# Kernel optimization log

Hardware: AMD Instinct MI355X
Metric: run time of the kernel (lower is better)

Reference implementation:

```python
import jax, jax.numpy as jnp
import numpy as np

B, C_IN, N = 128, 256, 1024
C_OUT = 256
L = 3069  # 3 * (N - 1) triplet indices, multiple of kernel_size=3


def setup_inputs() -> dict:
    key = jax.random.key(0)
    k1, k2, k3, k4 = jax.random.split(key, 4)
    data = jax.random.normal(k1, (B, C_IN, N), dtype=jnp.float32)
    indexes = jax.random.randint(k2, (B, L, 1), 0, N, dtype=jnp.int64)
    # Conv1d(in_dims, out_dims, kernel_size=3) params, PyTorch layout [out, in, k]
    fan_in = C_IN * 3
    bound = 1.0 / np.sqrt(fan_in)
    weight = jax.random.uniform(k3, (C_OUT, C_IN, 3), dtype=jnp.float32, minval=-bound, maxval=bound)
    bias = jax.random.uniform(k4, (C_OUT,), dtype=jnp.float32, minval=-bound, maxval=bound)
    return {"data": data, "indexes": indexes, "weight": weight, "bias": bias}


def reference(data, indexes, weight, bias):
    # gather: data[b, c, indexes[b, l, 0]] -> [B, C_IN, L]
    idx = indexes[:, :, 0]  # [B, L]
    gathered = jnp.take_along_axis(data, idx[:, None, :], axis=2)  # broadcast over channel dim
    # Conv1d kernel_size=3 stride=3 == per-triplet matmul:
    # reshape [B, C_IN, L] -> [B, C_IN, L//3, 3]; contract with weight [C_OUT, C_IN, 3]
    trip = gathered.reshape(B, gathered.shape[1], L // 3, 3)
    feats = jnp.einsum('bcnk,ock->bon', trip, weight) + bias[None, :, None]  # [B, C_OUT, L//3]
    # prepend a zero column (padding slot for node index 0)
    zeros = jnp.zeros((feats.shape[0], feats.shape[1], 1), dtype=feats.dtype)
    feats = jnp.concatenate((zeros, feats), axis=2)  # [B, C_OUT, L//3 + 1]
    return (feats, indexes)
```

## Files before the change

### kernel.cpp

```cpp
#include <hip/hip_runtime.h>

#define B_      128
#define C_IN_   256
#define NPTS    1024
#define C_OUT_  256
#define L_      3069
#define NTRIP   1023
#define T_OUT   1024
#define FEATS_SIZE (B_ * C_OUT_ * T_OUT)
#define KTOT    768

#define BK      96
#define NCHUNK  8
#define THREADS 512

typedef __attribute__((ext_vector_type(8))) short           bf16x8;
typedef __attribute__((ext_vector_type(8))) unsigned short  ushort8;
typedef __attribute__((ext_vector_type(4))) unsigned short  ushort4v;
typedef __attribute__((ext_vector_type(4))) float           f32x4;

__device__ __forceinline__ unsigned short f2bf(float f) {
    union { float f; unsigned u; } v; v.f = f;
    unsigned r = (v.u + 0x7FFFu + ((v.u >> 16) & 1u)) >> 16;
    return (unsigned short)r;
}

#define WOFF_T  0
#define DOFF_T  393216
#define WS_NEED_T2 (393216 + 67108864)

#define IDX3    32768
#define SMEM3   34304
#define BN2     128

__global__ __launch_bounds__(256) void convert_w3(
    const float* __restrict__ w, unsigned short* __restrict__ wbf3)
{
    int i = blockIdx.x * 256 + threadIdx.x;
    if (i >= C_OUT_ * KTOT) return;
    int j   = i & 7;
    int lgv = (i >> 3) & 3;
    int row = (i >> 5) & 255;
    int c   = i >> 13;
    int ks  = c % 3;
    int kc  = c / 3;
    int korig = (kc * 32 + lgv * 8 + j) * 3 + ks;
    wbf3[i] = f2bf(w[row * KTOT + korig]);
}

__global__ __launch_bounds__(256) void transpose_data(
    const float* __restrict__ data, unsigned short* __restrict__ dataT)
{
    __shared__ float T[64][68];
    const int bid = blockIdx.x;
    const int b   = bid >> 6;
    const int ct  = (bid & 63) >> 4;
    const int nt  = bid & 15;
    const int c0  = ct * 64, n0 = nt * 64;
    const int t   = threadIdx.x;
    const int row = t >> 2;
    const int q   = t & 3;

    const float* src = data + ((size_t)(b * C_IN_ + c0 + row)) * NPTS + n0 + q * 16;
    #pragma unroll
    for (int j = 0; j < 4; ++j) {
        float4 v = *(const float4*)(src + j * 4);
        *(float4*)&T[row][q * 16 + j * 4] = v;
    }
    __syncthreads();

    ushort8 o0, o1;
    #pragma unroll
    for (int j = 0; j < 8; ++j)  o0[j] = f2bf(T[q * 16 + j][row]);
    #pragma unroll
    for (int j = 0; j < 8; ++j)  o1[j] = f2bf(T[q * 16 + 8 + j][row]);
    unsigned short* dst = dataT + ((size_t)(b * NPTS) + n0 + row) * C_IN_ + c0 + q * 16;
    *(ushort8*)(dst)     = o0;
    *(ushort8*)(dst + 8) = o1;
}

__global__ __launch_bounds__(THREADS, 4) void treeconv_mfma3(
    const unsigned short* __restrict__ wbf3,
    const unsigned short* __restrict__ dataT,
    const int*   __restrict__ indexes,
    const float* __restrict__ bias,
    float*       __restrict__ out)
{
    __shared__ alignas(16) unsigned char smem[SMEM3];
    int* idx_s = (int*)(smem + IDX3);

    const int tid = threadIdx.x;
    const int b   = blockIdx.x >> 3;
    const int nt0 = (blockIdx.x & 7) * BN2;

    if (tid < BN2 * 3) {
        int off = nt0 * 3 + tid;
        idx_s[tid] = (off < L_) ? indexes[b * L_ + off] : 0;
    }
    __syncthreads();

    const int lane = tid & 63;
    const int wid  = tid >> 6;
    const int wm   = wid >> 1;
    const int wn   = wid & 1;
    const int l15  = lane & 15;
    const int lg   = lane >> 4;

    unsigned boff[4];
    #pragma unroll
    for (int j = 0; j < 4; ++j) {
        int slot = wid * 256 + j * 64 + lane;
        int n    = slot >> 4;
        int el   = (slot & 15) ^ (n & 7);
        int tap  = (el < 12) ? (el >> 2) : 0;
        int q    = el & 3;
        int ix   = idx_s[n * 3 + tap];
        boff[j]  = (unsigned)(ix * (C_IN_ * 2) + q * 16);
    }

    const char* dTb  = (const char*)dataT + (size_t)b * NPTS * C_IN_ * 2;
    const char* wsrc = (const char*)wbf3;
    const int   aoff = wm * 4096 + l15 * 64 + lg * 16;
    unsigned char* bdst = smem + wid * 4096 + lane * 16;

    f32x4 acc[4][4];
    #pragma unroll
    for (int mi = 0; mi < 4; ++mi)
        #pragma unroll
        for (int ni = 0; ni < 4; ++ni)
            acc[mi][ni] = (f32x4){0.f, 0.f, 0.f, 0.f};

    f32x4 breg[4];
    #pragma unroll
    for (int j = 0; j < 4; ++j)
        breg[j] = *(const f32x4*)(dTb + boff[j]);

    for (int kc = 0; kc < NCHUNK; ++kc) {
        __syncthreads();
        #pragma unroll
        for (int j = 0; j < 4; ++j)
            *(f32x4*)(bdst + j * 1024) = breg[j];
        __syncthreads();

        if (kc + 1 < NCHUNK) {
            #pragma unroll
            for (int j = 0; j < 4; ++j)
                breg[j] = *(const f32x4*)(dTb + (kc + 1) * 64 + boff[j]);
        }

        const char* wchunk = wsrc + kc * 49152;
        #pragma unroll
        for (int ks = 0; ks < 3; ++ks) {
            bf16x8 a[4];
            #pragma unroll
            for (int mi = 0; mi < 4; ++mi)
                a[mi] = *(const bf16x8*)(wchunk + ks * 16384 + mi * 1024 + aoff);
            const int kb = ks * 64 + lg * 16;
            bf16x8 bb[4];
            #pragma unroll
            for (int ni = 0; ni < 4; ++ni) {
                int row = wn * 64 + ni * 16 + l15;
                bb[ni] = *(const bf16x8*)(smem + row * 256 + (kb ^ ((row & 7) << 4)));
            }
            #pragma unroll
            for (int mi = 0; mi < 4; ++mi)
                #pragma unroll
                for (int ni = 0; ni < 4; ++ni)
                    acc[mi][ni] = __builtin_amdgcn_mfma_f32_16x16x32_bf16(
                        a[mi], bb[ni], acc[mi][ni], 0, 0, 0);
        }
    }

    float* outB = out + (size_t)b * (C_OUT_ * T_OUT);
    #pragma unroll
    for (int mi = 0; mi < 4; ++mi) {
        #pragma unroll
        for (int r = 0; r < 4; ++r) {
            int o = wm * 64 + mi * 16 + lg * 4 + r;
            float bv = bias[o];
            #pragma unroll
            for (int ni = 0; ni < 4; ++ni) {
                int n = nt0 + wn * 64 + ni * 16 + l15;
                if (n < NTRIP)
                    outB[o * T_OUT + 1 + n] = acc[mi][ni][r] + bv;
            }
        }
    }
}

#define BN      64
#define AS_OFF  0
#define BS_OFF  49152
#define IDX_OFF 61440
#define SMEM_BYTES 62208

template<bool PREW>
__global__ __launch_bounds__(THREADS, 4) void treeconv_mfma(
    const float* __restrict__ data,
    const int*   __restrict__ indexes,
    const float* __restrict__ w32,
    const unsigned short* __restrict__ wbf,
    const float* __restrict__ bias,
    float*       __restrict__ out)
{
    __shared__ alignas(16) unsigned char smem[SMEM_BYTES];
    int* idx_s = (int*)(smem + IDX_OFF);

    const int tid = threadIdx.x;
    const int b   = blockIdx.x >> 4;
    const int nt0 = (blockIdx.x & 15) * BN;

    if (tid < BN * 3) {
        int off = nt0 * 3 + tid;
        idx_s[tid] = (off < L_) ? indexes[b * L_ + off] : 0;
    }
    __syncthreads();

    const int lane = tid & 63;
    const int wid  = tid >> 6;
    const int wm   = wid >> 1;
    const int wn   = wid & 1;
    const int l15  = lane & 15;
    const int lg   = lane >> 4;

    f32x4 acc[4][2];
    #pragma unroll
    for (int mi = 0; mi < 4; ++mi)
        #pragma unroll
        for (int ni = 0; ni < 2; ++ni)
            acc[mi][ni] = (f32x4){0.f, 0.f, 0.f, 0.f};

    const float* dataB = data + (size_t)b * (C_IN_ * NPTS);
    const int ar = tid >> 1;
    const int ah = tid & 1;
    const int gn = tid & 63;
    const int g8 = tid >> 6;

    for (int kc = 0; kc < NCHUNK; ++kc) {
        {
            const int ab = ar * 192 + ah * 96;
            const int sw = (ar & 7) << 4;
            if (PREW) {
                const ushort8* src = (const ushort8*)(wbf + ar * KTOT + kc * BK + ah * 48);
                #pragma unroll
                for (int j = 0; j < 6; ++j) {
                    ushort8 v = src[j];
                    *(ushort8*)(smem + ((ab + j * 16) ^ sw)) = v;
                }
            } else {
                const float* src = w32 + ar * KTOT + kc * BK + ah * 48;
                #pragma unroll
                for (int j = 0; j < 6; ++j) {
                    float4 fa = *(const float4*)(src + j * 8);
                    float4 fb = *(const float4*)(src + j * 8 + 4);
                    ushort8 v;
                    v[0] = f2bf(fa.x); v[1] = f2bf(fa.y); v[2] = f2bf(fa.z); v[3] = f2bf(fa.w);
                    v[4] = f2bf(fb.x); v[5] = f2bf(fb.y); v[6] = f2bf(fb.z); v[7] = f2bf(fb.w);
                    *(ushort8*)(smem + ((ab + j * 16) ^ sw)) = v;
                }
            }
        }
        {
            const int* ip = idx_s + gn * 3;
            int ix0 = ip[0], ix1 = ip[1], ix2 = ip[2];
            const float* dp = dataB + (kc * 32 + g8 * 4) * NPTS;
            unsigned short vals[12];
            #pragma unroll
            for (int ci = 0; ci < 4; ++ci) {
                vals[ci * 3 + 0] = f2bf(dp[ix0]);
                vals[ci * 3 + 1] = f2bf(dp[ix1]);
                vals[ci * 3 + 2] = f2bf(dp[ix2]);
                dp += NPTS;
            }
            const int bb = BS_OFF + gn * 192 + g8 * 24;
            const int sw = (gn & 7) << 4;
            #pragma unroll
            for (int q = 0; q < 3; ++q) {
                ushort4v v;
                v[0] = vals[q * 4 + 0]; v[1] = vals[q * 4 + 1];
                v[2] = vals[q * 4 + 2]; v[3] = vals[q * 4 + 3];
                *(ushort4v*)(smem + ((bb + q * 8) ^ sw)) = v;
            }
        }
        __syncthreads();

        #pragma unroll
        for (int ks = 0; ks < 3; ++ks) {
            bf16x8 a[4], bf[2];
            const int kb = ks * 64 + lg * 16;
            #pragma unroll
            for (int mi = 0; mi < 4; ++mi) {
                int row = wm * 64 + mi * 16 + l15;
                a[mi] = *(const bf16x8*)(smem + ((row * 192 + kb) ^ ((row & 7) << 4)));
            }
            #pragma unroll
            for (int ni = 0; ni < 2; ++ni) {
                int row = wn * 32 + ni * 16 + l15;
                bf[ni] = *(const bf16x8*)(smem + ((BS_OFF + row * 192 + kb) ^ ((row & 7) << 4)));
            }
            #pragma unroll
            for (int mi = 0; mi < 4; ++mi)
                #pragma unroll
                for (int ni = 0; ni < 2; ++ni)
                    acc[mi][ni] = __builtin_amdgcn_mfma_f32_16x16x32_bf16(
                        a[mi], bf[ni], acc[mi][ni], 0, 0, 0);
        }
        __syncthreads();
    }

    float* outB = out + (size_t)b * (C_OUT_ * T_OUT);
    #pragma unroll
    for (int mi = 0; mi < 4; ++mi) {
        #pragma unroll
        for (int r = 0; r < 4; ++r) {
            int o = wm * 64 + mi * 16 + lg * 4 + r;
            float bv = bias[o];
            #pragma unroll
            for (int ni = 0; ni < 2; ++ni) {
                int n = nt0 + wn * 32 + ni * 16 + l15;
                if (n < NTRIP)
                    outB[o * T_OUT + 1 + n] = acc[mi][ni][r] + bv;
            }
        }
    }
}

__global__ __launch_bounds__(256) void convert_w(
    const float* __restrict__ w, unsigned short* __restrict__ wbf)
{
    int i = (blockIdx.x * 256 + threadIdx.x) * 4;
    if (i < C_OUT_ * KTOT) {
        float4 f = *(const float4*)(w + i);
        ushort4v v;
        v[0] = f2bf(f.x); v[1] = f2bf(f.y); v[2] = f2bf(f.z); v[3] = f2bf(f.w);
        *(ushort4v*)(wbf + i) = v;
    }
}

__global__ __launch_bounds__(256) void aux_kernel(
    const int* __restrict__ indexes, float* __restrict__ out)
{
    int i = blockIdx.x * 256 + threadIdx.x;
    if (i < B_ * L_)
        out[FEATS_SIZE + i] = (float)indexes[i];
    if (i < B_ * C_OUT_)
        out[(size_t)i * T_OUT] = 0.0f;
}

extern "C" void kernel_launch(void* const* d_in, const int* in_sizes, int n_in,
                              void* d_out, int out_size, void* d_ws, size_t ws_size,
                              hipStream_t stream)
{
    const float* data    = (const float*)d_in[0];
    const int*   indexes = (const int*)d_in[1];
    const float* weight  = (const float*)d_in[2];
    const float* bias    = (const float*)d_in[3];
    float* out = (float*)d_out;

    hipLaunchKernelGGL(aux_kernel, dim3((B_ * L_ + 255) / 256), dim3(256), 0, stream,
                       indexes, out);

    if (ws_size >= (size_t)WS_NEED_T2) {
        unsigned short* wbf3  = (unsigned short*)((char*)d_ws + WOFF_T);
        unsigned short* dataT = (unsigned short*)((char*)d_ws + DOFF_T);
        hipLaunchKernelGGL(convert_w3, dim3((C_OUT_ * KTOT + 255) / 256), dim3(256),
                           0, stream, weight, wbf3);
        hipLaunchKernelGGL(transpose_data, dim3(B_ * 64), dim3(256), 0, stream,
                           data, dataT);
        hipLaunchKernelGGL(treeconv_mfma3, dim3(B_ * 8), dim3(THREADS), 0, stream,
                           wbf3, dataT, indexes, bias, out);
    } else if (ws_size >= (size_t)(C_OUT_ * KTOT * 2)) {
        unsigned short* wbf = (unsigned short*)d_ws;
        hipLaunchKernelGGL(convert_w, dim3((C_OUT_ * KTOT / 4 + 255) / 256), dim3(256),
                           0, stream, weight, wbf);
        hipLaunchKernelGGL((treeconv_mfma<true>), dim3(B_ * 16), dim3(THREADS), 0, stream,
                           data, indexes, weight, wbf, bias, out);
    } else {
        hipLaunchKernelGGL((treeconv_mfma<false>), dim3(B_ * 16), dim3(THREADS), 0, stream,
                           data, indexes, weight, (const unsigned short*)d_ws, bias, out);
    }
}
```

Measured before the change: 143.8 us.

## Triple-buffer A and B tiles via direct global-to-LDS loads in MFMA GEMM

Rewrites the main gather-GEMM kernel so that both the bf16 weight slices and the gathered data rows are streamed into LDS with global_load_lds in a three-buffer ring, two slices ahead. Waits use explicit vmcnt counts and there is one barrier per slice. The weight layout is re-swizzled so the A operand is read from LDS rather than straight from global memory. Block indices are remapped so that neighbouring blocks work on different batches. The aim is to overlap the memory latency of the gather with MFMA work and to remove register staging and the double barrier, at the cost of more LDS per block (about 72KB), which may lower occupancy.

```diff
diff --git a/kernel.cpp b/kernel.cpp
--- a/kernel.cpp
+++ b/kernel.cpp
@@ -10,8 +10,6 @@
 #define FEATS_SIZE (B_ * C_OUT_ * T_OUT)
 #define KTOT    768
 
-#define BK      96
-#define NCHUNK  8
 #define THREADS 512
 
 typedef __attribute__((ext_vector_type(8))) short           bf16x8;
@@ -25,27 +23,38 @@
     return (unsigned short)r;
 }
 
+__device__ __forceinline__ void gload16(const void* g, void* l) {
+    __builtin_amdgcn_global_load_lds(
+        (const __attribute__((address_space(1))) unsigned int*)g,
+        (__attribute__((address_space(3))) unsigned int*)l, 16, 0, 0);
+}
+
 #define WOFF_T  0
 #define DOFF_T  393216
 #define WS_NEED_T2 (393216 + 67108864)
 
-#define IDX3    32768
-#define SMEM3   34304
+#define NSLICE  24
+#define ABYTES  16384
+#define BBYTES  8192
+#define BUFSZ   (ABYTES + BBYTES)
+#define SMEM4   (3 * BUFSZ)
+#define IDX4    (2 * BUFSZ)
 #define BN2     128
 
-__global__ __launch_bounds__(256) void convert_w3(
-    const float* __restrict__ w, unsigned short* __restrict__ wbf3)
+__global__ __launch_bounds__(256) void convert_w4(
+    const float* __restrict__ w, unsigned short* __restrict__ wbf4)
 {
     int i = blockIdx.x * 256 + threadIdx.x;
     if (i >= C_OUT_ * KTOT) return;
-    int j   = i & 7;
-    int lgv = (i >> 3) & 3;
-    int row = (i >> 5) & 255;
-    int c   = i >> 13;
-    int ks  = c % 3;
-    int kc  = c / 3;
-    int korig = (kc * 32 + lgv * 8 + j) * 3 + ks;
-    wbf3[i] = f2bf(w[row * KTOT + korig]);
+    int e  = i & 7;
+    int j  = (i >> 3) & 3;
+    int r  = (i >> 5) & 255;
+    int s  = i >> 13;
+    int t  = s >> 3;
+    int cb = s & 7;
+    int lgp = j ^ (r & 3);
+    int c  = cb * 32 + lgp * 8 + e;
+    wbf4[i] = f2bf(w[r * KTOT + c * 3 + t]);
 }
 
 __global__ __launch_bounds__(256) void transpose_data(
@@ -79,19 +88,20 @@
     *(ushort8*)(dst + 8) = o1;
 }
 
-__global__ __launch_bounds__(THREADS, 4) void treeconv_mfma3(
-    const unsigned short* __restrict__ wbf3,
+__global__ __launch_bounds__(THREADS, 4) void treeconv_mfma4(
+    const unsigned short* __restrict__ wbf4,
     const unsigned short* __restrict__ dataT,
     const int*   __restrict__ indexes,
     const float* __restrict__ bias,
     float*       __restrict__ out)
 {
-    __shared__ alignas(16) unsigned char smem[SMEM3];
-    int* idx_s = (int*)(smem + IDX3);
+    __shared__ alignas(16) unsigned char smem[SMEM4];
+    int* idx_s = (int*)(smem + IDX4);
 
     const int tid = threadIdx.x;
-    const int b   = blockIdx.x >> 3;
-    const int nt0 = (blockIdx.x & 7) * BN2;
+    const int wg  = (blockIdx.x & 7) * 128 + (blockIdx.x >> 3);
+    const int b   = wg >> 3;
+    const int nt0 = (wg & 7) * BN2;
 
     if (tid < BN2 * 3) {
         int off = nt0 * 3 + tid;
@@ -106,22 +116,21 @@
     const int l15  = lane & 15;
     const int lg   = lane >> 4;
 
-    unsigned boff[4];
-    #pragma unroll
-    for (int j = 0; j < 4; ++j) {
-        int slot = wid * 256 + j * 64 + lane;
-        int n    = slot >> 4;
-        int el   = (slot & 15) ^ (n & 7);
-        int tap  = (el < 12) ? (el >> 2) : 0;
-        int q    = el & 3;
-        int ix   = idx_s[n * 3 + tap];
-        boff[j]  = (unsigned)(ix * (C_IN_ * 2) + q * 16);
-    }
+    const int slotB = wid * 64 + lane;
+    const int nB    = slotB >> 2;
+    const int lgp   = (slotB & 3) ^ (nB & 3);
+    const unsigned boff0 = (unsigned)(idx_s[nB * 3 + 0] * 512 + lgp * 16);
+    const unsigned boff1 = (unsigned)(idx_s[nB * 3 + 1] * 512 + lgp * 16);
+    const unsigned boff2 = (unsigned)(idx_s[nB * 3 + 2] * 512 + lgp * 16);
+    const int bdst = ABYTES + slotB * 16;
 
     const char* dTb  = (const char*)dataT + (size_t)b * NPTS * C_IN_ * 2;
-    const char* wsrc = (const char*)wbf3;
-    const int   aoff = wm * 4096 + l15 * 64 + lg * 16;
-    unsigned char* bdst = smem + wid * 4096 + lane * 16;
+    const char* wsrc = (const char*)wbf4;
+    const int   a0   = (wid * 128 + lane) * 16;
+
+    const unsigned xsl   = (unsigned)((lg ^ (l15 & 3)) << 4);
+    const unsigned abase = (unsigned)((wm * 64 + l15) * 64) + xsl;
+    const unsigned bbase = (unsigned)(ABYTES + (wn * 64 + l15) * 64) + xsl;
 
     f32x4 acc[4][4];
     #pragma unroll
@@ -130,46 +139,43 @@
         for (int ni = 0; ni < 4; ++ni)
             acc[mi][ni] = (f32x4){0.f, 0.f, 0.f, 0.f};
 
-    f32x4 breg[4];
-    #pragma unroll
-    for (int j = 0; j < 4; ++j)
-        breg[j] = *(const f32x4*)(dTb + boff[j]);
-
-    for (int kc = 0; kc < NCHUNK; ++kc) {
-        __syncthreads();
-        #pragma unroll
-        for (int j = 0; j < 4; ++j)
-            *(f32x4*)(bdst + j * 1024) = breg[j];
-        __syncthreads();
-
-        if (kc + 1 < NCHUNK) {
-            #pragma unroll
-            for (int j = 0; j < 4; ++j)
-                breg[j] = *(const f32x4*)(dTb + (kc + 1) * 64 + boff[j]);
-        }
-
-        const char* wchunk = wsrc + kc * 49152;
-        #pragma unroll
-        for (int ks = 0; ks < 3; ++ks) {
-            bf16x8 a[4];
-            #pragma unroll
-            for (int mi = 0; mi < 4; ++mi)
-                a[mi] = *(const bf16x8*)(wchunk + ks * 16384 + mi * 1024 + aoff);
-            const int kb = ks * 64 + lg * 16;
-            bf16x8 bb[4];
-            #pragma unroll
-            for (int ni = 0; ni < 4; ++ni) {
-                int row = wn * 64 + ni * 16 + l15;
-                bb[ni] = *(const bf16x8*)(smem + row * 256 + (kb ^ ((row & 7) << 4)));
-            }
-            #pragma unroll
-            for (int mi = 0; mi < 4; ++mi)
-                #pragma unroll
-                for (int ni = 0; ni < 4; ++ni)
-                    acc[mi][ni] = __builtin_amdgcn_mfma_f32_16x16x32_bf16(
-                        a[mi], bb[ni], acc[mi][ni], 0, 0, 0);
-        }
-    }
+#define STAGE4(s, buf) do {                                                   \
+        gload16(wsrc + (s) * ABYTES + a0,        smem + (buf) * BUFSZ + a0);  \
+        gload16(wsrc + (s) * ABYTES + a0 + 1024, smem + (buf) * BUFSZ + a0 + 1024); \
+        unsigned bo = (((s) >> 3) == 0 ? boff0 : ((s) >> 3) == 1 ? boff1 : boff2) \
+                      + (unsigned)(((s) & 7) * 64);                           \
+        gload16(dTb + bo, smem + (buf) * BUFSZ + bdst);                       \
+    } while (0)
+
+    STAGE4(0, 0);
+    STAGE4(1, 1);
+
+    #pragma unroll
+    for (int s = 0; s < NSLICE; ++s) {
+        if (s == NSLICE - 1) asm volatile("s_waitcnt vmcnt(0)" ::: "memory");
+        else                 asm volatile("s_waitcnt vmcnt(3)" ::: "memory");
+        __builtin_amdgcn_s_barrier();
+        asm volatile("" ::: "memory");
+
+        const unsigned char* bufp = smem + (s % 3) * BUFSZ;
+        bf16x8 a[4], bb[4];
+        #pragma unroll
+        for (int mi = 0; mi < 4; ++mi)
+            a[mi] = *(const bf16x8*)(bufp + abase + mi * 1024);
+        #pragma unroll
+        for (int ni = 0; ni < 4; ++ni)
+            bb[ni] = *(const bf16x8*)(bufp + bbase + ni * 1024);
+
+        if (s + 2 < NSLICE) STAGE4(s + 2, (s + 2) % 3);
+
+        #pragma unroll
+        for (int mi = 0; mi < 4; ++mi)
+            #pragma unroll
+            for (int ni = 0; ni < 4; ++ni)
+                acc[mi][ni] = __builtin_amdgcn_mfma_f32_16x16x32_bf16(
+                    a[mi], bb[ni], acc[mi][ni], 0, 0, 0);
+    }
+#undef STAGE4
 
     float* outB = out + (size_t)b * (C_OUT_ * T_OUT);
     #pragma unroll
@@ -189,6 +195,8 @@
 }
 
 #define BN      64
+#define BK      96
+#define NCHUNK  8
 #define AS_OFF  0
 #define BS_OFF  49152
 #define IDX_OFF 61440
@@ -361,14 +369,14 @@
                        indexes, out);
 
     if (ws_size >= (size_t)WS_NEED_T2) {
-        unsigned short* wbf3  = (unsigned short*)((char*)d_ws + WOFF_T);
+        unsigned short* wbf4  = (unsigned short*)((char*)d_ws + WOFF_T);
         unsigned short* dataT = (unsigned short*)((char*)d_ws + DOFF_T);
-        hipLaunchKernelGGL(convert_w3, dim3((C_OUT_ * KTOT + 255) / 256), dim3(256),
-                           0, stream, weight, wbf3);
+        hipLaunchKernelGGL(convert_w4, dim3((C_OUT_ * KTOT + 255) / 256), dim3(256),
+                           0, stream, weight, wbf4);
         hipLaunchKernelGGL(transpose_data, dim3(B_ * 64), dim3(256), 0, stream,
                            data, dataT);
-        hipLaunchKernelGGL(treeconv_mfma3, dim3(B_ * 8), dim3(THREADS), 0, stream,
-                           wbf3, dataT, indexes, bias, out);
+        hipLaunchKernelGGL(treeconv_mfma4, dim3(B_ * 8), dim3(THREADS), 0, stream,
+                           wbf4, dataT, indexes, bias, out);
     } else if (ws_size >= (size_t)(C_OUT_ * KTOT * 2)) {
         unsigned short* wbf = (unsigned short*)d_ws;
         hipLaunchKernelGGL(convert_w, dim3((C_OUT_ * KTOT / 4 + 255) / 256), dim3(256),
```

Result: faster. 116.5 us (-19.0%).
